# Kernel tuning notes

Hardware: AMD Instinct MI355X
Metric: run time of the kernel (lower is better)

The kernel has to match this reference:

```python
import jax, jax.numpy as jnp
import numpy as np

POOLER_SIZE = 56
SPATIAL_SCALE = 0.25
B, P, K, H, W, A = 4, 512, 4, 200, 336, 14
IMG_H, IMG_W = H / SPATIAL_SCALE, W / SPATIAL_SCALE


def _roi_align_one(feat, boxes):
    """torchvision RoIAlign (aligned=False, sampling_ratio=1).
    feat: [K, H, W]; boxes: [P, 4] as (x1, y1, x2, y2) in image coords.
    Returns [P, K, ps, ps]."""
    Kc, Hf, Wf = feat.shape
    ps = POOLER_SIZE
    s = SPATIAL_SCALE
    x1 = boxes[:, 0] * s
    y1 = boxes[:, 1] * s
    x2 = boxes[:, 2] * s
    y2 = boxes[:, 3] * s
    rw = jnp.maximum(x2 - x1, 1.0)  # non-aligned mode clamps roi size to >= 1
    rh = jnp.maximum(y2 - y1, 1.0)
    bw = rw / ps
    bh = rh / ps
    grid = jnp.arange(ps, dtype=feat.dtype) + 0.5  # sampling_ratio=1 -> bin center
    xs = x1[:, None] + grid[None, :] * bw[:, None]  # [P, ps]
    ys = y1[:, None] + grid[None, :] * bh[:, None]  # [P, ps]
    xx = jnp.broadcast_to(xs[:, None, :], (xs.shape[0], ps, ps))  # [P, ps, ps]
    yy = jnp.broadcast_to(ys[:, :, None], (ys.shape[0], ps, ps))
    valid = (yy > -1.0) & (yy < Hf) & (xx > -1.0) & (xx < Wf)
    y = jnp.clip(yy, 0.0, Hf - 1)
    x = jnp.clip(xx, 0.0, Wf - 1)
    y0 = jnp.floor(y).astype(jnp.int32)
    x0 = jnp.floor(x).astype(jnp.int32)
    y1i = jnp.minimum(y0 + 1, Hf - 1)
    x1i = jnp.minimum(x0 + 1, Wf - 1)
    ly = y - y0
    lx = x - x0
    f = feat.reshape(Kc, Hf * Wf)

    def gather(yi, xi):
        idx = (yi * Wf + xi).reshape(-1)
        return jnp.take(f, idx, axis=1).reshape((Kc,) + yi.shape)  # [K, P, ps, ps]

    w00 = ((1.0 - ly) * (1.0 - lx))[None]
    w01 = ((1.0 - ly) * lx)[None]
    w10 = (ly * (1.0 - lx))[None]
    w11 = (ly * lx)[None]
    v = (gather(y0, x0) * w00 + gather(y0, x1i) * w01 +
         gather(y1i, x0) * w10 + gather(y1i, x1i) * w11)
    v = v * valid[None].astype(feat.dtype)
    return jnp.transpose(v, (1, 0, 2, 3))  # [P, K, ps, ps]


def _bilinear_resize_ac(x, ps):
    """F.interpolate(mode='bilinear', align_corners=True) on last two dims (square a->ps)."""
    a = x.shape[-1]
    src = jnp.arange(ps, dtype=x.dtype) * ((a - 1) / (ps - 1))
    i0 = jnp.clip(jnp.floor(src).astype(jnp.int32), 0, a - 2)
    i1 = i0 + 1
    t = src - i0.astype(x.dtype)
    rows = x[..., i0, :] * (1.0 - t)[:, None] + x[..., i1, :] * t[:, None]  # [..., ps, a]
    out = rows[..., :, i0] * (1.0 - t) + rows[..., :, i1] * t  # [..., ps, ps]
    return out


def setup_inputs() -> dict:
    key = jax.random.key(0)
    k1, k2, k3, k4, k5, k6 = jax.random.split(key, 6)
    bases = jax.random.normal(k1, (B, K, H, W), dtype=jnp.float32)
    attention_proposals = jax.random.normal(k2, (B, P, K, A, A), dtype=jnp.float32)
    # realistic boxes inside an 800x1344 image
    x1 = jax.random.uniform(k3, (B, P)) * (IMG_W - 64.0)
    y1 = jax.random.uniform(k4, (B, P)) * (IMG_H - 64.0)
    bw = 32.0 + jax.random.uniform(k5, (B, P)) * 256.0
    bh = 32.0 + jax.random.uniform(k6, (B, P)) * 256.0
    x2 = jnp.minimum(x1 + bw, IMG_W)
    y2 = jnp.minimum(y1 + bh, IMG_H)
    box_proposals = jnp.stack([x1, y1, x2, y2], axis=-1).astype(jnp.float32)  # [B, P, 4]
    return {"bases": bases, "box_proposals": box_proposals,
            "attention_proposals": attention_proposals}


def reference(bases, box_proposals, attention_proposals):
    ps = POOLER_SIZE
    rois = jax.vmap(_roi_align_one)(bases, box_proposals)  # [B, P, K, ps, ps]
    attn = _bilinear_resize_ac(attention_proposals, ps)    # [B, P, K, ps, ps]
    attn = jax.nn.softmax(attn, axis=2)                    # softmax over num_bases
    return (attn * rois).sum(axis=2)                       # [B, P, ps, ps]
```

## Files before the change

### kernel.cpp

```cpp
#include <hip/hip_runtime.h>
#include <math.h>

#define B_  4
#define P_  512
#define K_  4
#define H_  200
#define W_  336
#define A_  14
#define PS_ 56
#define SCALE_ 0.25f
#define HWB_ (H_ * W_ * 4)
#define APS_ (A_ * PS_)

#if __has_builtin(__builtin_amdgcn_exp2f)
#define EXP2F(x) __builtin_amdgcn_exp2f(x)
#else
#define EXP2F(x) exp2f(x)
#endif

__global__ __launch_bounds__(256) void blender_kernel(
    const float* __restrict__ bases,
    const float* __restrict__ boxes,
    const float* __restrict__ attn,
    float* __restrict__ out)
{
    const int tid = threadIdx.x;
    const int bp  = blockIdx.x;
    const int b   = bp >> 9;

    __shared__ float  smTile[K_ * A_ * A_];
    __shared__ float  smR[K_ * APS_];
    __shared__ float4 smX[PS_];
    __shared__ float4 smY[PS_];
    __shared__ float2 smAY[PS_];

    const float* ap = attn + (size_t)bp * (K_ * A_ * A_);
    for (int i = tid; i < K_ * A_ * A_; i += 256)
        smTile[i] = __builtin_nontemporal_load(ap + i);

    const float* bx = boxes + (size_t)bp * 4;
    const float rr = 13.0f / 55.0f;

    if (tid < PS_) {
        const int px = tid;
        const float x1 = bx[0] * SCALE_;
        const float x2 = bx[2] * SCALE_;
        const float bw = fmaxf(x2 - x1, 1.0f) * (1.0f / PS_);
        const float sx = x1 + (px + 0.5f) * bw;
        const float vx = (sx > -1.0f && sx < (float)W_) ? 1.0f : 0.0f;
        const float cx = fminf(fmaxf(sx, 0.0f), (float)(W_ - 1));
        const int   x0 = (int)cx;
        const int   x1i = min(x0 + 1, W_ - 1);
        const float lx = cx - (float)x0;
        float4 v;
        v.x = __int_as_float(x0 * 4);
        v.y = __int_as_float((x1i - x0) * 4);
        v.z = lx * vx;
        v.w = (1.0f - lx) * vx;
        smX[px] = v;
    } else if (tid >= 64 && tid < 64 + PS_) {
        const int py = tid - 64;
        const float y1 = bx[1] * SCALE_;
        const float y2 = bx[3] * SCALE_;
        const float bh = fmaxf(y2 - y1, 1.0f) * (1.0f / PS_);
        const float sy = y1 + (py + 0.5f) * bh;
        const float vy = (sy > -1.0f && sy < (float)H_) ? 1.0f : 0.0f;
        const float cy = fminf(fmaxf(sy, 0.0f), (float)(H_ - 1));
        const int   y0 = (int)cy;
        const int   y1i = min(y0 + 1, H_ - 1);
        const float ly = cy - (float)y0;
        float4 v;
        v.x = __int_as_float(y0 * (W_ * 4));
        v.y = __int_as_float((y1i - y0) * (W_ * 4));
        v.z = ly * vy;
        v.w = (1.0f - ly) * vy;
        smY[py] = v;
        const float srcy = (float)py * rr;
        const int iy0 = min((int)srcy, A_ - 2);
        float2 a;
        a.x = __int_as_float(iy0 * PS_);
        a.y = srcy - (float)iy0;
        smAY[py] = a;
    }
    __syncthreads();

    const float LOG2E = 1.4426950408889634f;
    for (int i = tid; i < K_ * APS_; i += 256) {
        const int k  = i / APS_;
        const int r1 = i - k * APS_;
        const int ay = r1 / PS_;
        const int px = r1 - ay * PS_;
        const float srcx = (float)px * rr;
        const int ix0 = min((int)srcx, A_ - 2);
        const float tx = srcx - (float)ix0;
        const float* t = smTile + k * (A_ * A_) + ay * A_ + ix0;
        smR[i] = (t[0] + tx * (t[1] - t[0])) * LOG2E;
    }
    __syncthreads();

    const char* fb = (const char*)(bases + (size_t)b * (K_ * H_ * W_));
    float* outp = out + (size_t)bp * (PS_ * PS_);

    auto prep = [&](int idx, int* o, float* w, const float*& rb, float& ty) {
        const int py = idx / PS_;
        const int px = idx - py * PS_;
        const float4 X = smX[px];
        const float4 Y = smY[py];
        const float2 AY = smAY[py];
        const int o00 = __float_as_int(Y.x) + __float_as_int(X.x);
        const int dx  = __float_as_int(X.y);
        const int dy  = __float_as_int(Y.y);
        o[0] = o00;      o[1] = o00 + dx;
        o[2] = o00 + dy; o[3] = o00 + dy + dx;
        w[0] = Y.w * X.w; w[1] = Y.w * X.z;
        w[2] = Y.z * X.w; w[3] = Y.z * X.z;
        rb = smR + __float_as_int(AY.x) + px;
        ty = AY.y;
    };
    auto issue = [&](const int* o, float* g) {
        #pragma unroll
        for (int k = 0; k < K_; ++k) {
            const char* f = fb + k * HWB_;
            #pragma unroll
            for (int c = 0; c < 4; ++c)
                g[k * 4 + c] = *(const float*)(f + o[c]);
        }
    };
    auto finish = [&](const float* g, const float* w, const float* rb, float ty) -> float {
        const float ct = 1.0f - ty;
        float s = 0.0f, acc = 0.0f;
        #pragma unroll
        for (int k = 0; k < K_; ++k) {
            const float v = g[k*4+0] * w[0] + g[k*4+1] * w[1]
                          + g[k*4+2] * w[2] + g[k*4+3] * w[3];
            const float a0 = rb[k * APS_];
            const float a1 = rb[k * APS_ + PS_];
            const float e  = EXP2F(a0 * ct + a1 * ty);
            s += e;
            acc = fmaf(e, v, acc);
        }
        return acc * __builtin_amdgcn_rcpf(s);
    };

    int   oA[4], oB[4];
    float wA[4], wB[4];
    float gA[16], gB[16];
    const float *rbA, *rbB;
    float tyA, tyB;

    prep(tid, oA, wA, rbA, tyA);
    issue(oA, gA);

    #pragma unroll
    for (int g = 0; g < 12; g += 2) {
        prep(tid + (g + 1) * 256, oB, wB, rbB, tyB);
        issue(oB, gB);
        __builtin_nontemporal_store(finish(gA, wA, rbA, tyA), outp + tid + g * 256);

        if (g + 2 < 12) {
            prep(tid + (g + 2) * 256, oA, wA, rbA, tyA);
            issue(oA, gA);
        } else if (tid < 64) {
            prep(3072 + tid, oA, wA, rbA, tyA);
            issue(oA, gA);
        }
        __builtin_nontemporal_store(finish(gB, wB, rbB, tyB), outp + tid + (g + 1) * 256);
    }
    if (tid < 64)
        __builtin_nontemporal_store(finish(gA, wA, rbA, tyA), outp + 3072 + tid);
}

extern "C" void kernel_launch(void* const* d_in, const int* in_sizes, int n_in,
                              void* d_out, int out_size, void* d_ws, size_t ws_size,
                              hipStream_t stream) {
    const float* bases = (const float*)d_in[0];
    const float* boxes = (const float*)d_in[1];
    const float* attn  = (const float*)d_in[2];
    float* out = (float*)d_out;

    blender_kernel<<<dim3(B_ * P_), dim3(256), 0, stream>>>(bases, boxes, attn, out);
}
```

Measured before the change: 105.2 us.

## Use 448-thread blocks with float2 pair gathers and K-interleaved attention table

After: 96.70 us. 8.1% less time.

```diff
diff --git a/kernel.cpp b/kernel.cpp
--- a/kernel.cpp
+++ b/kernel.cpp
@@ -10,7 +10,8 @@
 #define PS_ 56
 #define SCALE_ 0.25f
 #define HWB_ (H_ * W_ * 4)
-#define APS_ (A_ * PS_)
+#define ROWB_ (W_ * 4)
+#define RROWB_ (PS_ * K_ * 4)
 
 #if __has_builtin(__builtin_amdgcn_exp2f)
 #define EXP2F(x) __builtin_amdgcn_exp2f(x)
@@ -18,7 +19,7 @@
 #define EXP2F(x) exp2f(x)
 #endif
 
-__global__ __launch_bounds__(256) void blender_kernel(
+__global__ __launch_bounds__(448) void blender_kernel(
     const float* __restrict__ bases,
     const float* __restrict__ boxes,
     const float* __restrict__ attn,
@@ -29,13 +30,13 @@
     const int b   = bp >> 9;
 
     __shared__ float  smTile[K_ * A_ * A_];
-    __shared__ float  smR[K_ * APS_];
+    __shared__ float  smR[A_ * PS_ * K_];
     __shared__ float4 smX[PS_];
     __shared__ float4 smY[PS_];
     __shared__ float2 smAY[PS_];
 
     const float* ap = attn + (size_t)bp * (K_ * A_ * A_);
-    for (int i = tid; i < K_ * A_ * A_; i += 256)
+    for (int i = tid; i < K_ * A_ * A_; i += 448)
         smTile[i] = __builtin_nontemporal_load(ap + i);
 
     const float* bx = boxes + (size_t)bp * 4;
@@ -50,13 +51,18 @@
         const float vx = (sx > -1.0f && sx < (float)W_) ? 1.0f : 0.0f;
         const float cx = fminf(fmaxf(sx, 0.0f), (float)(W_ - 1));
         const int   x0 = (int)cx;
-        const int   x1i = min(x0 + 1, W_ - 1);
         const float lx = cx - (float)x0;
         float4 v;
-        v.x = __int_as_float(x0 * 4);
-        v.y = __int_as_float((x1i - x0) * 4);
-        v.z = lx * vx;
-        v.w = (1.0f - lx) * vx;
+        if (x0 >= W_ - 1) {
+            v.x = __int_as_float((W_ - 2) * 4);
+            v.y = 0.0f;
+            v.z = vx;
+        } else {
+            v.x = __int_as_float(x0 * 4);
+            v.y = (1.0f - lx) * vx;
+            v.z = lx * vx;
+        }
+        v.w = 0.0f;
         smX[px] = v;
     } else if (tid >= 64 && tid < 64 + PS_) {
         const int py = tid - 64;
@@ -70,104 +76,76 @@
         const int   y1i = min(y0 + 1, H_ - 1);
         const float ly = cy - (float)y0;
         float4 v;
-        v.x = __int_as_float(y0 * (W_ * 4));
-        v.y = __int_as_float((y1i - y0) * (W_ * 4));
-        v.z = ly * vy;
-        v.w = (1.0f - ly) * vy;
+        v.x = __int_as_float(y0 * ROWB_);
+        v.y = __int_as_float((y1i - y0) * ROWB_);
+        v.z = (1.0f - ly) * vy;
+        v.w = ly * vy;
         smY[py] = v;
         const float srcy = (float)py * rr;
         const int iy0 = min((int)srcy, A_ - 2);
         float2 a;
-        a.x = __int_as_float(iy0 * PS_);
+        a.x = __int_as_float(iy0 * RROWB_);
         a.y = srcy - (float)iy0;
         smAY[py] = a;
     }
     __syncthreads();
 
     const float LOG2E = 1.4426950408889634f;
-    for (int i = tid; i < K_ * APS_; i += 256) {
-        const int k  = i / APS_;
-        const int r1 = i - k * APS_;
+    for (int i = tid; i < K_ * A_ * PS_; i += 448) {
+        const int k  = i / (A_ * PS_);
+        const int r1 = i - k * (A_ * PS_);
         const int ay = r1 / PS_;
         const int px = r1 - ay * PS_;
         const float srcx = (float)px * rr;
         const int ix0 = min((int)srcx, A_ - 2);
         const float tx = srcx - (float)ix0;
         const float* t = smTile + k * (A_ * A_) + ay * A_ + ix0;
-        smR[i] = (t[0] + tx * (t[1] - t[0])) * LOG2E;
+        smR[(ay * PS_ + px) * K_ + k] = (t[0] + tx * (t[1] - t[0])) * LOG2E;
     }
     __syncthreads();
 
     const char* fb = (const char*)(bases + (size_t)b * (K_ * H_ * W_));
     float* outp = out + (size_t)bp * (PS_ * PS_);
 
-    auto prep = [&](int idx, int* o, float* w, const float*& rb, float& ty) {
-        const int py = idx / PS_;
-        const int px = idx - py * PS_;
-        const float4 X = smX[px];
-        const float4 Y = smY[py];
+    const int px  = tid % PS_;
+    const int py0 = tid / PS_;
+
+    const float4 X = smX[px];
+    const unsigned xb = (unsigned)__float_as_int(X.x);
+    const float wl = X.y, wh = X.z;
+    const char* smRbase = (const char*)smR + (px << 4);
+
+    #pragma unroll
+    for (int t = 0; t < 7; ++t) {
+        const int py = py0 + 8 * t;
+        const float4 Y  = smY[py];
         const float2 AY = smAY[py];
-        const int o00 = __float_as_int(Y.x) + __float_as_int(X.x);
-        const int dx  = __float_as_int(X.y);
-        const int dy  = __float_as_int(Y.y);
-        o[0] = o00;      o[1] = o00 + dx;
-        o[2] = o00 + dy; o[3] = o00 + dy + dx;
-        w[0] = Y.w * X.w; w[1] = Y.w * X.z;
-        w[2] = Y.z * X.w; w[3] = Y.z * X.z;
-        rb = smR + __float_as_int(AY.x) + px;
-        ty = AY.y;
-    };
-    auto issue = [&](const int* o, float* g) {
+        const unsigned o0 = (unsigned)__float_as_int(Y.x) + xb;
+        const unsigned o1 = o0 + (unsigned)__float_as_int(Y.y);
+        const float wy0 = Y.z, wy1 = Y.w;
+        const float ty  = AY.y;
+
+        const float4 a0v = *(const float4*)(smRbase + __float_as_int(AY.x));
+        const float4 a1v = *(const float4*)(smRbase + __float_as_int(AY.x) + RROWB_);
+
+        float s = 0.0f, acc = 0.0f;
         #pragma unroll
         for (int k = 0; k < K_; ++k) {
             const char* f = fb + k * HWB_;
-            #pragma unroll
-            for (int c = 0; c < 4; ++c)
-                g[k * 4 + c] = *(const float*)(f + o[c]);
-        }
-    };
-    auto finish = [&](const float* g, const float* w, const float* rb, float ty) -> float {
-        const float ct = 1.0f - ty;
-        float s = 0.0f, acc = 0.0f;
-        #pragma unroll
-        for (int k = 0; k < K_; ++k) {
-            const float v = g[k*4+0] * w[0] + g[k*4+1] * w[1]
-                          + g[k*4+2] * w[2] + g[k*4+3] * w[3];
-            const float a0 = rb[k * APS_];
-            const float a1 = rb[k * APS_ + PS_];
-            const float e  = EXP2F(a0 * ct + a1 * ty);
+            const float2 r0 = *(const float2*)(f + o0);
+            const float2 r1 = *(const float2*)(f + o1);
+            const float rr0 = fmaf(r0.y, wh, r0.x * wl);
+            const float rr1 = fmaf(r1.y, wh, r1.x * wl);
+            const float v   = fmaf(rr1, wy1, rr0 * wy0);
+            const float a0  = (k == 0) ? a0v.x : (k == 1) ? a0v.y : (k == 2) ? a0v.z : a0v.w;
+            const float a1  = (k == 0) ? a1v.x : (k == 1) ? a1v.y : (k == 2) ? a1v.z : a1v.w;
+            const float e   = EXP2F(fmaf(ty, a1 - a0, a0));
             s += e;
             acc = fmaf(e, v, acc);
         }
-        return acc * __builtin_amdgcn_rcpf(s);
-    };
-
-    int   oA[4], oB[4];
-    float wA[4], wB[4];
-    float gA[16], gB[16];
-    const float *rbA, *rbB;
-    float tyA, tyB;
-
-    prep(tid, oA, wA, rbA, tyA);
-    issue(oA, gA);
-
-    #pragma unroll
-    for (int g = 0; g < 12; g += 2) {
-        prep(tid + (g + 1) * 256, oB, wB, rbB, tyB);
-        issue(oB, gB);
-        __builtin_nontemporal_store(finish(gA, wA, rbA, tyA), outp + tid + g * 256);
-
-        if (g + 2 < 12) {
-            prep(tid + (g + 2) * 256, oA, wA, rbA, tyA);
-            issue(oA, gA);
-        } else if (tid < 64) {
-            prep(3072 + tid, oA, wA, rbA, tyA);
-            issue(oA, gA);
-        }
-        __builtin_nontemporal_store(finish(gB, wB, rbB, tyB), outp + tid + (g + 1) * 256);
+        __builtin_nontemporal_store(acc * __builtin_amdgcn_rcpf(s),
+                                    outp + tid + 448 * t);
     }
-    if (tid < 64)
-        __builtin_nontemporal_store(finish(gA, wA, rbA, tyA), outp + 3072 + tid);
 }
 
 extern "C" void kernel_launch(void* const* d_in, const int* in_sizes, int n_in,
@@ -178,5 +156,5 @@
     const float* attn  = (const float*)d_in[2];
     float* out = (float*)d_out;
 
-    blender_kernel<<<dim3(B_ * P_), dim3(256), 0, stream>>>(bases, boxes, attn, out);
+    blender_kernel<<<dim3(B_ * P_), dim3(448), 0, stream>>>(bases, boxes, attn, out);
 }
```
